# Kernel optimization log

Hardware: AMD Instinct MI355X
Metric: run time of the kernel (lower is better)

## Reference

```python
import jax, jax.numpy as jnp
import numpy as np

B_SZ, D0, T = 64, 256, 2048   # batch, input feature dim, time dim
D1, D2 = 128, 3               # output_dim


def setup_inputs() -> dict:
    key = jax.random.key(0)
    ks = jax.random.split(key, 8)
    s = 0.02  # small init so softmax logits stay well-conditioned
    return {
        "X":       jax.random.normal(ks[0], (B_SZ, D0, T), dtype=jnp.float32),
        "W1":      jax.random.normal(ks[1], (D1, D0), dtype=jnp.float32) * s,
        "DFSMNW1": jax.random.normal(ks[2], (T, T), dtype=jnp.float32) * s,
        "DFSMNW2": jax.random.normal(ks[3], (T, T), dtype=jnp.float32) * s,
        "DFSMNW3": jax.random.normal(ks[4], (T, T), dtype=jnp.float32) * s,
        "DFSMNW4": jax.random.normal(ks[5], (T, T), dtype=jnp.float32) * s,
        "W2":      jax.random.normal(ks[6], (T, D2), dtype=jnp.float32) * s,
        "B":       jax.random.normal(ks[7], (D1, D2), dtype=jnp.float32) * s,
    }


def _dfsmn_stage(D, M_prev, W):
    # E = D @ W over time axis; legacy nn.Softmax() default for 3D input is dim=0.
    E = jnp.einsum('bot,ts->bos', D, W)
    A = jax.nn.softmax(E, axis=0)
    M = D * A + M_prev          # gated memory + running residual
    return D + M, M


def reference(X, W1, DFSMNW1, DFSMNW2, DFSMNW3, DFSMNW4, W2, B):
    # X_: [B, D1, T] = W1 @ X per sample
    X_ = jnp.einsum('od,bdt->bot', W1, X)

    # Stage 1 (no previous memory)
    A1 = jax.nn.softmax(jnp.einsum('bot,ts->bos', X_, DFSMNW1), axis=0)
    M1 = X_ * A1
    D_1 = X_ + M1

    D_2, M2 = _dfsmn_stage(D_1, M1, DFSMNW2)
    D_3, M3 = _dfsmn_stage(D_2, M2, DFSMNW3)
    D_4, _  = _dfsmn_stage(D_3, M3, DFSMNW4)

    # Output projection + bias: [B, D1, D2]
    Y = jnp.einsum('bot,td->bod', D_4, W2) + B
    return Y
```

## Files before the change

kernel.cpp:

```cpp
#include <hip/hip_runtime.h>

#define TT   2048
#define BSZ  64
#define DD0  256
#define DD1  128
#define DD2  3
#define NROW (DD1*BSZ)

typedef unsigned char u8;
typedef __attribute__((ext_vector_type(8))) short short8;
typedef __attribute__((ext_vector_type(4))) float f32x4;
typedef __attribute__((ext_vector_type(4))) unsigned short us4;
typedef __attribute__((ext_vector_type(4))) int i32x4;
typedef __attribute__((ext_vector_type(8))) int i32x8;

__device__ __forceinline__ unsigned short f2b(float f) {
  unsigned u = __builtin_bit_cast(unsigned, f);
  unsigned r = (u + 0x7fffu + ((u >> 16) & 1u)) >> 16;
  return (unsigned short)r;
}
__device__ __forceinline__ float b2f(unsigned short s) {
  unsigned u = ((unsigned)s) << 16;
  return __builtin_bit_cast(float, u);
}
__device__ __forceinline__ u8 f2f8(float x) {
  return (u8)(__builtin_amdgcn_cvt_pk_fp8_f32(x, 0.f, 0, false) & 0xff);
}
__device__ __forceinline__ unsigned f2f8x4(float a, float b, float c, float d) {
  int v = __builtin_amdgcn_cvt_pk_fp8_f32(a, b, 0, false);
  v = __builtin_amdgcn_cvt_pk_fp8_f32(c, d, v, true);
  return (unsigned)v;
}

__device__ __forceinline__ void gload16(const void* g, void* l) {
  __builtin_amdgcn_global_load_lds(
      (const __attribute__((address_space(1))) unsigned int*)(unsigned long long)g,
      (__attribute__((address_space(3))) unsigned int*)(unsigned int)(unsigned long long)l,
      16, 0, 0);
}

__global__ __launch_bounds__(256) void transpose_cvt(
    const float* __restrict__ src, unsigned short* __restrict__ dst,
    int R, int C, long sstride, long dstride)
{
  __shared__ float tile[64 * 65];
  const int z = blockIdx.z;
  src += (size_t)z * sstride;
  dst += (size_t)z * dstride;
  const int c0 = blockIdx.x * 64, r0 = blockIdx.y * 64;
  const int tid = threadIdx.x;
#pragma unroll
  for (int i = 0; i < 4; ++i) {
    int e = i * 256 + tid;
    int r = e >> 4, q = e & 15;
    float4 v = *(const float4*)&src[(size_t)(r0 + r) * C + c0 + q * 4];
    tile[r * 65 + q * 4 + 0] = v.x;
    tile[r * 65 + q * 4 + 1] = v.y;
    tile[r * 65 + q * 4 + 2] = v.z;
    tile[r * 65 + q * 4 + 3] = v.w;
  }
  __syncthreads();
#pragma unroll
  for (int i = 0; i < 4; ++i) {
    int e = i * 256 + tid;
    int c = e >> 4, q = e & 15;
    us4 o;
    o[0] = f2b(tile[(q * 4 + 0) * 65 + c]);
    o[1] = f2b(tile[(q * 4 + 1) * 65 + c]);
    o[2] = f2b(tile[(q * 4 + 2) * 65 + c]);
    o[3] = f2b(tile[(q * 4 + 3) * 65 + c]);
    *(us4*)&dst[(size_t)(c0 + c) * R + r0 + q * 4] = o;
  }
}

__global__ __launch_bounds__(256) void transpose_cvt8(
    const float* __restrict__ src, u8* __restrict__ dst)
{
  __shared__ float tile[64 * 65];
  const int c0 = blockIdx.x * 64, r0 = blockIdx.y * 64;
  const int tid = threadIdx.x;
#pragma unroll
  for (int i = 0; i < 4; ++i) {
    int e = i * 256 + tid;
    int r = e >> 4, q = e & 15;
    float4 v = *(const float4*)&src[(size_t)(r0 + r) * TT + c0 + q * 4];
    tile[r * 65 + q * 4 + 0] = v.x;
    tile[r * 65 + q * 4 + 1] = v.y;
    tile[r * 65 + q * 4 + 2] = v.z;
    tile[r * 65 + q * 4 + 3] = v.w;
  }
  __syncthreads();
#pragma unroll
  for (int i = 0; i < 4; ++i) {
    int e = i * 256 + tid;
    int c = e >> 4, q = e & 15;
    unsigned v = f2f8x4(tile[(q * 4 + 0) * 65 + c] * 8.f,
                        tile[(q * 4 + 1) * 65 + c] * 8.f,
                        tile[(q * 4 + 2) * 65 + c] * 8.f,
                        tile[(q * 4 + 3) * 65 + c] * 8.f);
    *(unsigned*)&dst[(size_t)(c0 + c) * TT + r0 + q * 4] = v;
  }
}

__global__ __launch_bounds__(256) void proj_kernel(
    const float* __restrict__ W1, const unsigned short* __restrict__ Xt,
    unsigned short* __restrict__ Dout, u8* __restrict__ D8)
{
  __shared__ __align__(16) unsigned short Al[128 * 72];
  __shared__ __align__(16) unsigned short Bl[128 * 64];
  const int tid = threadIdx.x;
  const int b = blockIdx.y, t0 = blockIdx.x * 128;
  const int w = tid >> 6, l = tid & 63;
  const unsigned short* XtB = Xt + ((size_t)b * TT + t0) * DD0;

  f32x4 acc[8][2];
#pragma unroll
  for (int m = 0; m < 8; ++m)
#pragma unroll
    for (int n = 0; n < 2; ++n) acc[m][n] = f32x4{0.f, 0.f, 0.f, 0.f};

  for (int k0 = 0; k0 < DD0; k0 += 64) {
#pragma unroll
    for (int i = 0; i < 4; ++i) {
      int u = i * 256 + tid;
      int row = u >> 3, cg = u & 7;
      const float* s = &W1[row * DD0 + k0 + cg * 8];
      float4 v0 = *(const float4*)s;
      float4 v1 = *(const float4*)(s + 4);
      short8 p;
      p[0] = f2b(v0.x); p[1] = f2b(v0.y); p[2] = f2b(v0.z); p[3] = f2b(v0.w);
      p[4] = f2b(v1.x); p[5] = f2b(v1.y); p[6] = f2b(v1.z); p[7] = f2b(v1.w);
      *(short8*)&Al[row * 72 + cg * 8] = p;
    }
#pragma unroll
    for (int c = 0; c < 4; ++c) {
      int ob = (w * 4 + c) * 1024;
      int off = ob + l * 16;
      int row = off >> 7, c16 = (off >> 4) & 7;
      gload16((const char*)XtB + ((size_t)row * DD0 + k0) * 2 + ((c16 ^ (row & 7)) * 16),
              (char*)Bl + ob);
    }
    __syncthreads();
#pragma unroll
    for (int kk = 0; kk < 2; ++kk) {
      const int q = l >> 4;
      short8 bfr[2];
#pragma unroll
      for (int n = 0; n < 2; ++n) {
        int row = w * 32 + n * 16 + (l & 15);
        int c16 = (kk * 4 + q) ^ (row & 7);
        bfr[n] = *(const short8*)&Bl[row * 64 + c16 * 8];
      }
#pragma unroll
      for (int m = 0; m < 8; ++m) {
        int row = m * 16 + (l & 15);
        short8 a = *(const short8*)&Al[row * 72 + (kk * 4 + q) * 8];
        acc[m][0] = __builtin_amdgcn_mfma_f32_16x16x32_bf16(a, bfr[0], acc[m][0], 0, 0, 0);
        acc[m][1] = __builtin_amdgcn_mfma_f32_16x16x32_bf16(a, bfr[1], acc[m][1], 0, 0, 0);
      }
    }
    __syncthreads();
  }
#pragma unroll
  for (int m = 0; m < 8; ++m)
#pragma unroll
    for (int n = 0; n < 2; ++n)
#pragma unroll
      for (int r = 0; r < 4; ++r) {
        int o = m * 16 + (l >> 4) * 4 + r;
        int t = t0 + w * 32 + n * 16 + (l & 15);
        size_t idx = (size_t)(o * BSZ + b) * TT + t;
        float v = acc[m][n][r];
        Dout[idx] = f2b(v);
        D8[idx] = f2f8(v * 8.f);
      }
}

template <int FIRST, int LAST>
__global__ __launch_bounds__(512, 2) void stage_kernel(
    const u8* __restrict__ Din8, const unsigned short* __restrict__ DinBf,
    const u8* __restrict__ Wt8, const unsigned short* DprevBf,
    unsigned short* DoutBf, u8* __restrict__ Dout8)
{
  __shared__ __align__(16) unsigned short lds[65536];
  char* ldsb = (char*)lds;
  const int tid = threadIdx.x, w = tid >> 6, l = tid & 63;
  const int wr = w >> 2, wc = w & 3;
  const int L = blockIdx.y * 8 + blockIdx.x;
  const int s0 = ((L >> 3) & 7) * 256;
  const int r0 = ((L & 7) * 4 + (L >> 6)) * 256;
  const u8* DinR = Din8 + (size_t)r0 * TT;
  const u8* WtR  = Wt8 + (size_t)s0 * TT;
  const int q4 = l >> 4;
  const int NT = TT / 128;

  f32x4 acc[8][4];
#pragma unroll
  for (int m = 0; m < 8; ++m)
#pragma unroll
    for (int n = 0; n < 4; ++n) acc[m][n] = f32x4{0.f, 0.f, 0.f, 0.f};

  auto STAGE = [&](int tau) {
    if (tau >= NT) return;
    const int k0 = tau * 128, buf = tau & 1;
    const int lrow = l >> 3;
    const int swz = ((l & 7) ^ lrow) << 4;
#pragma unroll
    for (int c = 0; c < 8; ++c) {
      int ch = w * 8 + c;
      const u8* base = (ch & 32) ? WtR : DinR;
      int cc = ch & 31;
      gload16(base + (size_t)(cc * 8 + lrow) * TT + k0 + swz,
              ldsb + ((ch & 32) ? 65536 : 0) + buf * 32768 + cc * 1024);
    }
  };
  auto LDA = [&](int buf, int ah, i32x8 (&ar)[4]) {
#pragma unroll
    for (int m = 0; m < 4; ++m) {
      int ra = ah * 128 + wr * 64 + m * 16 + (l & 15);
      const char* rowp = ldsb + buf * 32768 + ra * 128;
      i32x4 lo = *(const i32x4*)(rowp + (((q4 * 2 + 0) ^ (ra & 7)) * 16));
      i32x4 hi = *(const i32x4*)(rowp + (((q4 * 2 + 1) ^ (ra & 7)) * 16));
      ar[m] = __builtin_shufflevector(lo, hi, 0, 1, 2, 3, 4, 5, 6, 7);
    }
  };
  auto LDB = [&](int buf, int bh, i32x8 (&br)[2]) {
#pragma unroll
    for (int n = 0; n < 2; ++n) {
      int rb = bh * 128 + wc * 32 + n * 16 + (l & 15);
      const char* rowp = ldsb + 65536 + buf * 32768 + rb * 128;
      i32x4 lo = *(const i32x4*)(rowp + (((q4 * 2 + 0) ^ (rb & 7)) * 16));
      i32x4 hi = *(const i32x4*)(rowp + (((q4 * 2 + 1) ^ (rb & 7)) * 16));
      br[n] = __builtin_shufflevector(lo, hi, 0, 1, 2, 3, 4, 5, 6, 7);
    }
  };
  auto MM = [&](int ah, int bh, i32x8 (&ar)[4], i32x8 (&br)[2]) {
    __builtin_amdgcn_s_setprio(1);
#pragma unroll
    for (int m = 0; m < 4; ++m)
#pragma unroll
      for (int n = 0; n < 2; ++n)
        acc[ah * 4 + m][bh * 2 + n] =
            __builtin_amdgcn_mfma_scale_f32_16x16x128_f8f6f4(
                ar[m], br[n], acc[ah * 4 + m][bh * 2 + n],
                0, 0,
                0, 0x7f7f7f7f,
                0, 0x7f7f7f7f);
    __builtin_amdgcn_s_setprio(0);
  };

  i32x8 a[4], b0[2], b1[2];

  STAGE(0);
  asm volatile("s_waitcnt vmcnt(0)" ::: "memory");
  __builtin_amdgcn_s_barrier();

#pragma unroll 1
  for (int t = 0; t < NT; ++t) {
    const int buf = t & 1;
    STAGE(t + 1);
    LDB(buf, 0, b0);
    LDA(buf, 0, a);
    LDB(buf, 1, b1);
    MM(0, 0, a, b0);
    MM(0, 1, a, b1);
    LDA(buf, 1, a);
    MM(1, 1, a, b1);
    MM(1, 0, a, b0);
    asm volatile("s_waitcnt vmcnt(0)" ::: "memory");
    __builtin_amdgcn_s_barrier();
  }

  const int cc = l & 15;
#pragma unroll
  for (int j = 0; j < 4; ++j) {
    const int bh = j >> 1, nn = j & 1;
    const int col = bh * 128 + wc * 32 + nn * 16 + cc;
    const int u = col >> 3;
#pragma unroll
    for (int ah = 0; ah < 2; ++ah) {
      float mx = -3.0e38f;
#pragma unroll
      for (int m = 0; m < 4; ++m)
#pragma unroll
        for (int r = 0; r < 4; ++r) mx = fmaxf(mx, acc[ah * 4 + m][j][r]);
      mx = fmaxf(mx, __shfl_xor(mx, 16));
      mx = fmaxf(mx, __shfl_xor(mx, 32));
      float pr[4][4];
      float sm = 0.f;
#pragma unroll
      for (int m = 0; m < 4; ++m)
#pragma unroll
        for (int r = 0; r < 4; ++r) {
          pr[m][r] = __expf((acc[ah * 4 + m][j][r] - mx) * 0.015625f);
          sm += pr[m][r];
        }
      sm += __shfl_xor(sm, 16);
      sm += __shfl_xor(sm, 32);
      const float rs = 1.f / sm;
#pragma unroll
      for (int m = 0; m < 4; ++m)
#pragma unroll
        for (int r = 0; r < 4; ++r) {
          int row = ah * 128 + wr * 64 + m * 16 + q4 * 4 + r;
          lds[row * 256 + (((u ^ ((row >> 2) & 7)) << 3) | (col & 7))] = f2b(pr[m][r] * rs);
        }
    }
  }
  asm volatile("s_waitcnt lgkmcnt(0)" ::: "memory");
  __builtin_amdgcn_s_barrier();

#pragma unroll 4
  for (int i = 0; i < 16; ++i) {
    int unit = i * 512 + tid;
    int row = unit >> 5, u = unit & 31;
    short8 a8 = *(const short8*)&lds[row * 256 + ((u ^ ((row >> 2) & 7)) << 3)];
    size_t g = (size_t)(r0 + row) * TT + s0 + u * 8;
    short8 d8 = *(const short8*)&DinBf[g];
    short8 dp8 = {};
    if (!FIRST) dp8 = *(const short8*)&DprevBf[g];
    short8 ob;
    float dn[8];
#pragma unroll
    for (int j = 0; j < 8; ++j) {
      float d = b2f((unsigned short)d8[j]);
      float aa = b2f((unsigned short)a8[j]);
      float mp = FIRST ? 0.f : (d - b2f((unsigned short)dp8[j]));
      float mn = fmaf(d, aa, mp);
      dn[j] = d + mn;
      ob[j] = (short)f2b(dn[j]);
    }
    *(short8*)&DoutBf[g] = ob;
    if (!LAST) {
      unsigned w0 = f2f8x4(dn[0] * 8.f, dn[1] * 8.f, dn[2] * 8.f, dn[3] * 8.f);
      unsigned w1 = f2f8x4(dn[4] * 8.f, dn[5] * 8.f, dn[6] * 8.f, dn[7] * 8.f);
      *(unsigned long long*)&Dout8[g] = (unsigned long long)w0 |
                                        ((unsigned long long)w1 << 32);
    }
  }
}

__global__ __launch_bounds__(256) void out_proj(
    const unsigned short* __restrict__ D4, const float* __restrict__ W2,
    const float* __restrict__ Bb, float* __restrict__ Y)
{
  const int r = blockIdx.x;
  const int o = r >> 6, b = r & 63;
  const int tid = threadIdx.x;
  float p0 = 0.f, p1 = 0.f, p2 = 0.f;
  for (int t = tid; t < TT; t += 256) {
    float d = b2f(D4[(size_t)r * TT + t]);
    p0 = fmaf(d, W2[t * 3 + 0], p0);
    p1 = fmaf(d, W2[t * 3 + 1], p1);
    p2 = fmaf(d, W2[t * 3 + 2], p2);
  }
#pragma unroll
  for (int off = 1; off < 64; off <<= 1) {
    p0 += __shfl_xor(p0, off);
    p1 += __shfl_xor(p1, off);
    p2 += __shfl_xor(p2, off);
  }
  __shared__ float red[4][3];
  const int w = tid >> 6, l = tid & 63;
  if (l == 0) { red[w][0] = p0; red[w][1] = p1; red[w][2] = p2; }
  __syncthreads();
  if (tid < 3) {
    float s = red[0][tid] + red[1][tid] + red[2][tid] + red[3][tid];
    Y[(size_t)(b * DD1 + o) * DD2 + tid] = s + Bb[o * DD2 + tid];
  }
}

extern "C" void kernel_launch(void* const* d_in, const int* in_sizes, int n_in,
                              void* d_out, int out_size, void* d_ws, size_t ws_size,
                              hipStream_t stream)
{
  const float* X  = (const float*)d_in[0];
  const float* W1 = (const float*)d_in[1];
  const float* DW[4] = {(const float*)d_in[2], (const float*)d_in[3],
                        (const float*)d_in[4], (const float*)d_in[5]};
  const float* W2 = (const float*)d_in[6];
  const float* Bb = (const float*)d_in[7];
  float* Y = (float*)d_out;

  u8* wsb = (u8*)d_ws;
  u8* Wt8[4];
  for (int i = 0; i < 4; ++i) Wt8[i] = wsb + (size_t)i * TT * TT;
  unsigned short* Dbf0 = (unsigned short*)(wsb + (16ull << 20));
  u8*             D80  = wsb + (48ull << 20);
  unsigned short* Dbf1 = (unsigned short*)(wsb + (64ull << 20));
  u8*             D81  = wsb + (96ull << 20);
  unsigned short* Xt   = (unsigned short*)(wsb + (64ull << 20));

  dim3 blk(256);
  for (int i = 0; i < 4; ++i)
    transpose_cvt8<<<dim3(TT / 64, TT / 64), blk, 0, stream>>>(DW[i], Wt8[i]);
  transpose_cvt<<<dim3(TT / 64, DD0 / 64, BSZ), blk, 0, stream>>>(
      X, Xt, DD0, TT, (long)DD0 * TT, (long)TT * DD0);

  proj_kernel<<<dim3(TT / 128, BSZ), blk, 0, stream>>>(W1, Xt, Dbf0, D80);

  dim3 sblk(512);
  dim3 sgrid(TT / 256, NROW / 256);
  stage_kernel<1, 0><<<sgrid, sblk, 0, stream>>>(D80, Dbf0, Wt8[0], Dbf0, Dbf1, D81);
  stage_kernel<0, 0><<<sgrid, sblk, 0, stream>>>(D81, Dbf1, Wt8[1], Dbf0, Dbf0, D80);
  stage_kernel<0, 0><<<sgrid, sblk, 0, stream>>>(D80, Dbf0, Wt8[2], Dbf1, Dbf1, D81);
  stage_kernel<0, 1><<<sgrid, sblk, 0, stream>>>(D81, Dbf1, Wt8[3], Dbf0, Dbf0, D80);

  out_proj<<<dim3(NROW), blk, 0, stream>>>(Dbf0, W2, Bb, Y);
}
```

Before: 304.0 us.

## Drop X transpose pass and fuse output projection into last stage epilogue

Removes the separate X transpose/bf16 conversion kernel: the projection now reads fp32 X directly with strided loads per k and keeps all of W1 in LDS (swizzled), dropping the per-k-chunk barriers. The final output projection kernel is also removed. Its dot with W2 is done in the last stage's epilogue with shuffle reductions and atomicAdd into Y, which a small init kernel pre-fills with the bias, and the last stage skips writing D4. The strided global reads of X in the projection may be less efficient than the old LDS-staged path, and atomics make the summation order nondeterministic.

```diff
diff --git a/kernel.cpp b/kernel.cpp
--- a/kernel.cpp
+++ b/kernel.cpp
@@ -37,40 +37,6 @@
       (const __attribute__((address_space(1))) unsigned int*)(unsigned long long)g,
       (__attribute__((address_space(3))) unsigned int*)(unsigned int)(unsigned long long)l,
       16, 0, 0);
-}
-
-__global__ __launch_bounds__(256) void transpose_cvt(
-    const float* __restrict__ src, unsigned short* __restrict__ dst,
-    int R, int C, long sstride, long dstride)
-{
-  __shared__ float tile[64 * 65];
-  const int z = blockIdx.z;
-  src += (size_t)z * sstride;
-  dst += (size_t)z * dstride;
-  const int c0 = blockIdx.x * 64, r0 = blockIdx.y * 64;
-  const int tid = threadIdx.x;
-#pragma unroll
-  for (int i = 0; i < 4; ++i) {
-    int e = i * 256 + tid;
-    int r = e >> 4, q = e & 15;
-    float4 v = *(const float4*)&src[(size_t)(r0 + r) * C + c0 + q * 4];
-    tile[r * 65 + q * 4 + 0] = v.x;
-    tile[r * 65 + q * 4 + 1] = v.y;
-    tile[r * 65 + q * 4 + 2] = v.z;
-    tile[r * 65 + q * 4 + 3] = v.w;
-  }
-  __syncthreads();
-#pragma unroll
-  for (int i = 0; i < 4; ++i) {
-    int e = i * 256 + tid;
-    int c = e >> 4, q = e & 15;
-    us4 o;
-    o[0] = f2b(tile[(q * 4 + 0) * 65 + c]);
-    o[1] = f2b(tile[(q * 4 + 1) * 65 + c]);
-    o[2] = f2b(tile[(q * 4 + 2) * 65 + c]);
-    o[3] = f2b(tile[(q * 4 + 3) * 65 + c]);
-    *(us4*)&dst[(size_t)(c0 + c) * R + r0 + q * 4] = o;
-  }
 }
 
 __global__ __launch_bounds__(256) void transpose_cvt8(
@@ -103,15 +69,28 @@
 }
 
 __global__ __launch_bounds__(256) void proj_kernel(
-    const float* __restrict__ W1, const unsigned short* __restrict__ Xt,
+    const float* __restrict__ W1, const float* __restrict__ X,
     unsigned short* __restrict__ Dout, u8* __restrict__ D8)
 {
-  __shared__ __align__(16) unsigned short Al[128 * 72];
-  __shared__ __align__(16) unsigned short Bl[128 * 64];
+  __shared__ __align__(16) unsigned short Al[128 * 256];
   const int tid = threadIdx.x;
   const int b = blockIdx.y, t0 = blockIdx.x * 128;
   const int w = tid >> 6, l = tid & 63;
-  const unsigned short* XtB = Xt + ((size_t)b * TT + t0) * DD0;
+  const int q4 = l >> 4;
+
+#pragma unroll
+  for (int i = 0; i < 16; ++i) {
+    int id = i * 256 + tid;
+    int row = id >> 5, u = id & 31;
+    const float* s = &W1[row * DD0 + u * 8];
+    float4 v0 = *(const float4*)s;
+    float4 v1 = *(const float4*)(s + 4);
+    short8 p;
+    p[0] = f2b(v0.x); p[1] = f2b(v0.y); p[2] = f2b(v0.z); p[3] = f2b(v0.w);
+    p[4] = f2b(v1.x); p[5] = f2b(v1.y); p[6] = f2b(v1.z); p[7] = f2b(v1.w);
+    *(short8*)&Al[row * 256 + ((u ^ (row & 7)) * 8)] = p;
+  }
+  __syncthreads();
 
   f32x4 acc[8][2];
 #pragma unroll
@@ -119,47 +98,26 @@
 #pragma unroll
     for (int n = 0; n < 2; ++n) acc[m][n] = f32x4{0.f, 0.f, 0.f, 0.f};
 
-  for (int k0 = 0; k0 < DD0; k0 += 64) {
-#pragma unroll
-    for (int i = 0; i < 4; ++i) {
-      int u = i * 256 + tid;
-      int row = u >> 3, cg = u & 7;
-      const float* s = &W1[row * DD0 + k0 + cg * 8];
-      float4 v0 = *(const float4*)s;
-      float4 v1 = *(const float4*)(s + 4);
+#pragma unroll 2
+  for (int kk = 0; kk < 8; ++kk) {
+    const int koff = kk * 32 + q4 * 8;
+    short8 bfr[2];
+#pragma unroll
+    for (int n = 0; n < 2; ++n) {
+      const int t = t0 + w * 32 + n * 16 + (l & 15);
+      const float* xp = X + (size_t)(b * DD0 + koff) * TT + t;
       short8 p;
-      p[0] = f2b(v0.x); p[1] = f2b(v0.y); p[2] = f2b(v0.z); p[3] = f2b(v0.w);
-      p[4] = f2b(v1.x); p[5] = f2b(v1.y); p[6] = f2b(v1.z); p[7] = f2b(v1.w);
-      *(short8*)&Al[row * 72 + cg * 8] = p;
-    }
-#pragma unroll
-    for (int c = 0; c < 4; ++c) {
-      int ob = (w * 4 + c) * 1024;
-      int off = ob + l * 16;
-      int row = off >> 7, c16 = (off >> 4) & 7;
-      gload16((const char*)XtB + ((size_t)row * DD0 + k0) * 2 + ((c16 ^ (row & 7)) * 16),
-              (char*)Bl + ob);
-    }
-    __syncthreads();
-#pragma unroll
-    for (int kk = 0; kk < 2; ++kk) {
-      const int q = l >> 4;
-      short8 bfr[2];
-#pragma unroll
-      for (int n = 0; n < 2; ++n) {
-        int row = w * 32 + n * 16 + (l & 15);
-        int c16 = (kk * 4 + q) ^ (row & 7);
-        bfr[n] = *(const short8*)&Bl[row * 64 + c16 * 8];
-      }
-#pragma unroll
-      for (int m = 0; m < 8; ++m) {
-        int row = m * 16 + (l & 15);
-        short8 a = *(const short8*)&Al[row * 72 + (kk * 4 + q) * 8];
-        acc[m][0] = __builtin_amdgcn_mfma_f32_16x16x32_bf16(a, bfr[0], acc[m][0], 0, 0, 0);
-        acc[m][1] = __builtin_amdgcn_mfma_f32_16x16x32_bf16(a, bfr[1], acc[m][1], 0, 0, 0);
-      }
-    }
-    __syncthreads();
+#pragma unroll
+      for (int j = 0; j < 8; ++j) p[j] = f2b(xp[(size_t)j * TT]);
+      bfr[n] = p;
+    }
+#pragma unroll
+    for (int m = 0; m < 8; ++m) {
+      int row = m * 16 + (l & 15);
+      short8 a = *(const short8*)&Al[row * 256 + (((kk * 4 + q4) ^ (row & 7)) * 8)];
+      acc[m][0] = __builtin_amdgcn_mfma_f32_16x16x32_bf16(a, bfr[0], acc[m][0], 0, 0, 0);
+      acc[m][1] = __builtin_amdgcn_mfma_f32_16x16x32_bf16(a, bfr[1], acc[m][1], 0, 0, 0);
+    }
   }
 #pragma unroll
   for (int m = 0; m < 8; ++m)
@@ -167,7 +125,7 @@
     for (int n = 0; n < 2; ++n)
 #pragma unroll
       for (int r = 0; r < 4; ++r) {
-        int o = m * 16 + (l >> 4) * 4 + r;
+        int o = m * 16 + q4 * 4 + r;
         int t = t0 + w * 32 + n * 16 + (l & 15);
         size_t idx = (size_t)(o * BSZ + b) * TT + t;
         float v = acc[m][n][r];
@@ -176,11 +134,19 @@
       }
 }
 
+__global__ __launch_bounds__(256) void init_y(
+    const float* __restrict__ Bb, float* __restrict__ Y)
+{
+  int id = blockIdx.x * 256 + threadIdx.x;
+  if (id < BSZ * DD1 * DD2) Y[id] = Bb[id % (DD1 * DD2)];
+}
+
 template <int FIRST, int LAST>
 __global__ __launch_bounds__(512, 2) void stage_kernel(
     const u8* __restrict__ Din8, const unsigned short* __restrict__ DinBf,
     const u8* __restrict__ Wt8, const unsigned short* DprevBf,
-    unsigned short* DoutBf, u8* __restrict__ Dout8)
+    unsigned short* DoutBf, u8* __restrict__ Dout8,
+    const float* __restrict__ W2, float* __restrict__ Y)
 {
   __shared__ __align__(16) unsigned short lds[65536];
   char* ldsb = (char*)lds;
@@ -243,9 +209,7 @@
         acc[ah * 4 + m][bh * 2 + n] =
             __builtin_amdgcn_mfma_scale_f32_16x16x128_f8f6f4(
                 ar[m], br[n], acc[ah * 4 + m][bh * 2 + n],
-                0, 0,
-                0, 0x7f7f7f7f,
-                0, 0x7f7f7f7f);
+                0, 0, 0, 0x7f7f7f7f, 0, 0x7f7f7f7f);
     __builtin_amdgcn_s_setprio(0);
   };
 
@@ -310,7 +274,7 @@
   asm volatile("s_waitcnt lgkmcnt(0)" ::: "memory");
   __builtin_amdgcn_s_barrier();
 
-#pragma unroll 4
+#pragma unroll 2
   for (int i = 0; i < 16; ++i) {
     int unit = i * 512 + tid;
     int row = unit >> 5, u = unit & 31;
@@ -322,51 +286,44 @@
     short8 ob;
     float dn[8];
 #pragma unroll
-    for (int j = 0; j < 8; ++j) {
-      float d = b2f((unsigned short)d8[j]);
-      float aa = b2f((unsigned short)a8[j]);
-      float mp = FIRST ? 0.f : (d - b2f((unsigned short)dp8[j]));
+    for (int jj = 0; jj < 8; ++jj) {
+      float d = b2f((unsigned short)d8[jj]);
+      float aa = b2f((unsigned short)a8[jj]);
+      float mp = FIRST ? 0.f : (d - b2f((unsigned short)dp8[jj]));
       float mn = fmaf(d, aa, mp);
-      dn[j] = d + mn;
-      ob[j] = (short)f2b(dn[j]);
-    }
-    *(short8*)&DoutBf[g] = ob;
+      dn[jj] = d + mn;
+      ob[jj] = (short)f2b(dn[jj]);
+    }
     if (!LAST) {
+      *(short8*)&DoutBf[g] = ob;
       unsigned w0 = f2f8x4(dn[0] * 8.f, dn[1] * 8.f, dn[2] * 8.f, dn[3] * 8.f);
       unsigned w1 = f2f8x4(dn[4] * 8.f, dn[5] * 8.f, dn[6] * 8.f, dn[7] * 8.f);
       *(unsigned long long*)&Dout8[g] = (unsigned long long)w0 |
                                         ((unsigned long long)w1 << 32);
-    }
-  }
-}
-
-__global__ __launch_bounds__(256) void out_proj(
-    const unsigned short* __restrict__ D4, const float* __restrict__ W2,
-    const float* __restrict__ Bb, float* __restrict__ Y)
-{
-  const int r = blockIdx.x;
-  const int o = r >> 6, b = r & 63;
-  const int tid = threadIdx.x;
-  float p0 = 0.f, p1 = 0.f, p2 = 0.f;
-  for (int t = tid; t < TT; t += 256) {
-    float d = b2f(D4[(size_t)r * TT + t]);
-    p0 = fmaf(d, W2[t * 3 + 0], p0);
-    p1 = fmaf(d, W2[t * 3 + 1], p1);
-    p2 = fmaf(d, W2[t * 3 + 2], p2);
-  }
-#pragma unroll
-  for (int off = 1; off < 64; off <<= 1) {
-    p0 += __shfl_xor(p0, off);
-    p1 += __shfl_xor(p1, off);
-    p2 += __shfl_xor(p2, off);
-  }
-  __shared__ float red[4][3];
-  const int w = tid >> 6, l = tid & 63;
-  if (l == 0) { red[w][0] = p0; red[w][1] = p1; red[w][2] = p2; }
-  __syncthreads();
-  if (tid < 3) {
-    float s = red[0][tid] + red[1][tid] + red[2][tid] + red[3][tid];
-    Y[(size_t)(b * DD1 + o) * DD2 + tid] = s + Bb[o * DD2 + tid];
+    } else {
+      float p0 = 0.f, p1 = 0.f, p2 = 0.f;
+#pragma unroll
+      for (int jj = 0; jj < 8; ++jj) {
+        const float* w2 = &W2[(size_t)(s0 + u * 8 + jj) * DD2];
+        p0 = fmaf(dn[jj], w2[0], p0);
+        p1 = fmaf(dn[jj], w2[1], p1);
+        p2 = fmaf(dn[jj], w2[2], p2);
+      }
+#pragma unroll
+      for (int off = 1; off < 32; off <<= 1) {
+        p0 += __shfl_xor(p0, off);
+        p1 += __shfl_xor(p1, off);
+        p2 += __shfl_xor(p2, off);
+      }
+      if ((l & 31) == 0) {
+        int gr = r0 + row;
+        int o = gr >> 6, bb = gr & 63;
+        float* y = &Y[(size_t)(bb * DD1 + o) * DD2];
+        atomicAdd(&y[0], p0);
+        atomicAdd(&y[1], p1);
+        atomicAdd(&y[2], p2);
+      }
+    }
   }
 }
 
@@ -389,22 +346,19 @@
   u8*             D80  = wsb + (48ull << 20);
   unsigned short* Dbf1 = (unsigned short*)(wsb + (64ull << 20));
   u8*             D81  = wsb + (96ull << 20);
-  unsigned short* Xt   = (unsigned short*)(wsb + (64ull << 20));
 
   dim3 blk(256);
   for (int i = 0; i < 4; ++i)
     transpose_cvt8<<<dim3(TT / 64, TT / 64), blk, 0, stream>>>(DW[i], Wt8[i]);
-  transpose_cvt<<<dim3(TT / 64, DD0 / 64, BSZ), blk, 0, stream>>>(
-      X, Xt, DD0, TT, (long)DD0 * TT, (long)TT * DD0);
-
-  proj_kernel<<<dim3(TT / 128, BSZ), blk, 0, stream>>>(W1, Xt, Dbf0, D80);
+
+  proj_kernel<<<dim3(TT / 128, BSZ), blk, 0, stream>>>(W1, X, Dbf0, D80);
+
+  init_y<<<dim3((BSZ * DD1 * DD2 + 255) / 256), blk, 0, stream>>>(Bb, Y);
 
   dim3 sblk(512);
   dim3 sgrid(TT / 256, NROW / 256);
-  stage_kernel<1, 0><<<sgrid, sblk, 0, stream>>>(D80, Dbf0, Wt8[0], Dbf0, Dbf1, D81);
-  stage_kernel<0, 0><<<sgrid, sblk, 0, stream>>>(D81, Dbf1, Wt8[1], Dbf0, Dbf0, D80);
-  stage_kernel<0, 0><<<sgrid, sblk, 0, stream>>>(D80, Dbf0, Wt8[2], Dbf1, Dbf1, D81);
-  stage_kernel<0, 1><<<sgrid, sblk, 0, stream>>>(D81, Dbf1, Wt8[3], Dbf0, Dbf0, D80);
-
-  out_proj<<<dim3(NROW), blk, 0, stream>>>(Dbf0, W2, Bb, Y);
-}
+  stage_kernel<1, 0><<<sgrid, sblk, 0, stream>>>(D80, Dbf0, Wt8[0], Dbf0, Dbf1, D81, W2, Y);
+  stage_kernel<0, 0><<<sgrid, sblk, 0, stream>>>(D81, Dbf1, Wt8[1], Dbf0, Dbf0, D80, W2, Y);
+  stage_kernel<0, 0><<<sgrid, sblk, 0, stream>>>(D80, Dbf0, Wt8[2], Dbf1, Dbf1, D81, W2, Y);
+  stage_kernel<0, 1><<<sgrid, sblk, 0, stream>>>(D81, Dbf1, Wt8[3], Dbf0, Dbf0, D80, W2, Y);
+}
```

Result: faster. 265.0 us, median of 3 (-12.8%).
